# Kernel tuning notes

Measured on AMD Instinct MI355X. Metric: run time of the kernel, lower is better.

The kernel has to match this reference:

```python
import jax, jax.numpy as jnp
import numpy as np

B, N, F, D, M, R, K, TOPR = 32, 1024, 10, 64, 4, 8, 20, 2
TAU = 1.0
BN_EPS = 1e-5


def setup_inputs() -> dict:
    key = jax.random.key(0)
    ks = jax.random.split(key, 20)
    s = 0.1
    p = {}
    p['data'] = jax.random.normal(ks[0], (B, N, F), jnp.float32)
    u = jnp.clip(jax.random.uniform(ks[1], (B, M), jnp.float32), 1e-6, 1.0 - 1e-6)
    p['gumbel_noise'] = -jnp.log(-jnp.log(u))
    p['W_cond'] = jax.random.normal(ks[2], (F, D), jnp.float32) * s
    p['b_cond'] = jnp.zeros((D,), jnp.float32)
    p['W_ap'] = jax.random.normal(ks[3], (D, D), jnp.float32) * s
    p['b_ap'] = jnp.zeros((D,), jnp.float32)
    p['W_av'] = jax.random.normal(ks[4], (D, 1), jnp.float32) * s
    p['W_r'] = jax.random.normal(ks[5], (D, M), jnp.float32) * s
    p['b_r'] = jnp.zeros((M,), jnp.float32)
    p['e_base'] = jax.random.normal(ks[6], (N, D), jnp.float32) * s
    p['lr_u'] = jax.random.normal(ks[7], (M, N, R), jnp.float32) * s
    p['lr_v'] = jax.random.normal(ks[8], (M, R, D), jnp.float32) * s
    p['W_gnn'] = jax.random.normal(ks[9], (F, D), jnp.float32) * s
    p['att_i'] = jax.random.normal(ks[10], (D,), jnp.float32) * s
    p['att_j'] = jax.random.normal(ks[11], (D,), jnp.float32) * s
    p['att_em_i'] = jax.random.normal(ks[12], (D,), jnp.float32) * s
    p['att_em_j'] = jax.random.normal(ks[13], (D,), jnp.float32) * s
    p['b_gnn'] = jnp.zeros((D,), jnp.float32)
    p['bn1_gamma'] = jnp.ones((D,), jnp.float32)
    p['bn1_beta'] = jnp.zeros((D,), jnp.float32)
    p['node_embed_table'] = jax.random.normal(ks[14], (N, D), jnp.float32) * s
    p['bn_out_gamma'] = jnp.ones((D,), jnp.float32)
    p['bn_out_beta'] = jnp.zeros((D,), jnp.float32)
    p['W_out'] = jax.random.normal(ks[15], (D, 1), jnp.float32) * s
    p['b_out'] = jnp.zeros((1,), jnp.float32)
    return p


def _nan(x):
    return jnp.nan_to_num(x, nan=0.0, posinf=1e4, neginf=-1e4)


def _bn(x, gamma, beta, axes):
    # BatchNorm1d in training mode: biased batch stats over `axes`.
    mu = x.mean(axes, keepdims=True)
    var = x.var(axes, keepdims=True)
    return (x - mu) * jax.lax.rsqrt(var + BN_EPS) * gamma + beta


def reference(data, gumbel_noise, W_cond, b_cond, W_ap, b_ap, W_av, W_r, b_r,
              e_base, lr_u, lr_v, W_gnn, att_i, att_j, att_em_i, att_em_j,
              b_gnn, bn1_gamma, bn1_beta, node_embed_table,
              bn_out_gamma, bn_out_beta, W_out, b_out):
    x_det = jax.lax.stop_gradient(data)                      # data.clone().detach()
    # --- condition attention pooling ---
    h_it = data @ W_cond + b_cond                            # [B,N,D]
    ah = jax.nn.leaky_relu(h_it @ W_ap + b_ap, 0.2)
    e_it = _nan((ah @ W_av)[..., 0])                         # [B,N]
    beta = jax.nn.softmax(e_it, axis=1)
    h_sys = jnp.sum(beta[..., None] * h_it, axis=1)          # [B,D]
    # --- gumbel top-k routing with straight-through ---
    pi_soft = jax.nn.softmax((h_sys @ W_r + b_r + gumbel_noise) / TAU, axis=-1)
    topv, topi = jax.lax.top_k(pi_soft, TOPR)
    pi_hard = jnp.sum(jax.nn.one_hot(topi, M, dtype=pi_soft.dtype) * topv[..., None], axis=1)
    pi_hard = pi_hard / jnp.maximum(pi_hard.sum(-1, keepdims=True), 1e-12)
    pi_t = jax.lax.stop_gradient(pi_hard - pi_soft) + pi_soft
    # --- low-rank expert prototypes -> mixed node embeddings ---
    proto = e_base[None] + jnp.einsum('mnr,mrd->mnd', lr_u, lr_v)    # [M,N,D]
    mixed = _nan(jnp.einsum('bm,mnd->bnd', pi_t, proto))             # [B,N,D]
    # --- dynamic top-k graph construction ---
    scores = _nan(jnp.einsum('bid,bjd->bij', mixed, mixed))          # [B,N,N]
    topk_vals, topk_idx = jax.lax.top_k(scores, K)                   # src nodes per dst: [B,N,K]
    topk_w = jax.nn.softmax(topk_vals, axis=-1)                      # edge weights
    # --- GAT-style layer with embedding-augmented keys, self loops re-added ---
    x_lin = x_det @ W_gnn                                            # [B,N,D]
    s_i = x_lin @ att_i + mixed @ att_em_i                           # [B,N]
    s_j = x_lin @ att_j + mixed @ att_em_j
    sj_nb = jnp.take_along_axis(s_j, topk_idx.reshape(B, N * K), axis=1).reshape(B, N, K)
    self_mask = topk_idx == jnp.arange(N)[None, :, None]             # remove_self_loops on topk edges
    alpha_nb = jnp.where(self_mask, -jnp.inf, jax.nn.leaky_relu(s_i[:, :, None] + sj_nb, 0.2))
    alpha_self = jax.nn.leaky_relu(s_i + s_j, 0.2)
    att = jax.nn.softmax(jnp.concatenate([alpha_nb, alpha_self[..., None]], axis=-1), axis=-1)
    w_nb = att[..., :K] * topk_w                                     # edge_weight modulation
    w_self = att[..., K]
    x_src = jnp.take_along_axis(x_lin, topk_idx.reshape(B, N * K)[..., None], axis=1).reshape(B, N, K, D)
    gnn = jnp.einsum('bnk,bnkd->bnd', w_nb, x_src) + w_self[..., None] * x_lin + b_gnn
    gnn = jax.nn.relu(_bn(gnn.reshape(B * N, D), bn1_gamma, bn1_beta, 0).reshape(B, N, D))
    # --- output head ---
    out = gnn * node_embed_table[None]                               # [B,N,D]
    out = jax.nn.relu(_bn(out, bn_out_gamma, bn_out_beta, (0, 1)))   # dropout = identity (eval)
    out = (out @ W_out + b_out).reshape(-1, N)                       # [B,N]
    return out, h_sys, pi_soft
```

## Files before the change

kernel.cpp:

```cpp
#include <hip/hip_runtime.h>
#include <math.h>

#define BB 32
#define NN 1024
#define FF 10
#define DD 64
#define MM 4
#define RR 8
#define KK 20
#define BNROWS (BB*NN)

#define OFF_HIT   0ull
#define OFF_XLIN  2097152ull
#define OFF_EIT   4194304ull
#define OFF_PIT   4227072ull
#define OFF_MIXED 4227200ull
#define OFF_SI    6324352ull
#define OFF_SJ    6357120ull
#define OFF_GNN   7700608ull
#define OFF_OUTP  9797760ull
#define OFF_STAT  11894912ull
#define OFF_SC    (OFF_STAT + 2560ull)

__device__ __forceinline__ float wave_sum(float v) {
    #pragma unroll
    for (int off = 32; off; off >>= 1) v += __shfl_xor(v, off);
    return v;
}
__device__ __forceinline__ float wave_max(float v) {
    #pragma unroll
    for (int off = 32; off; off >>= 1) v = fmaxf(v, __shfl_xor(v, off));
    return v;
}

__global__ __launch_bounds__(256) void k_rows(
    const float* __restrict__ data, const float* __restrict__ W_cond,
    const float* __restrict__ b_cond, const float* __restrict__ W_ap,
    const float* __restrict__ b_ap, const float* __restrict__ W_av,
    const float* __restrict__ W_gnn,
    float* __restrict__ h_it, float* __restrict__ x_lin, float* __restrict__ e_it,
    float* __restrict__ stats)
{
    if (blockIdx.x < 10) {
        int idx = blockIdx.x * 256 + threadIdx.x;
        if (idx < 2336) stats[idx] = 0.f;
    }
    int w = threadIdx.x >> 6, lane = threadIdx.x & 63;
    int r = blockIdx.x * 4 + w;
    const float* dr = data + r * FF;
    float df[FF];
    #pragma unroll
    for (int f = 0; f < FF; f++) df[f] = dr[f];
    float h = b_cond[lane], x = 0.f;
    #pragma unroll
    for (int f = 0; f < FF; f++) {
        h = fmaf(df[f], W_cond[f * DD + lane], h);
        x = fmaf(df[f], W_gnn[f * DD + lane], x);
    }
    h_it[r * DD + lane] = h;
    x_lin[r * DD + lane] = x;
    float acc = b_ap[lane];
    #pragma unroll
    for (int e2 = 0; e2 < DD; e2++)
        acc = fmaf(__shfl(h, e2), W_ap[e2 * DD + lane], acc);
    float lr = acc > 0.f ? acc : 0.2f * acc;
    float ep = wave_sum(lr * W_av[lane]);
    if (lane == 0) e_it[r] = ep;
}

__global__ __launch_bounds__(256) void k_pool2(
    const float* __restrict__ e_it, const float* __restrict__ h_it,
    float* __restrict__ num, float* __restrict__ den)
{
    int w = threadIdx.x >> 6, lane = threadIdx.x & 63;
    int b = blockIdx.x >> 3, ch = blockIdx.x & 7;
    int base = b * NN + ch * 128 + w * 32;
    float acc = 0.f, dn = 0.f;
    #pragma unroll 4
    for (int i = 0; i < 32; i++) {
        float e = e_it[base + i];
        float wgt = expf(e);
        acc = fmaf(wgt, h_it[(size_t)(base + i) * DD + lane], acc);
        dn += wgt;
    }
    __shared__ float pa[4][DD];
    __shared__ float pd[4];
    pa[w][lane] = acc;
    if (lane == 0) pd[w] = dn;
    __syncthreads();
    if (w == 0) {
        float s = pa[0][lane] + pa[1][lane] + pa[2][lane] + pa[3][lane];
        atomicAdd(&num[b * DD + lane], s);
        if (lane == 0) atomicAdd(&den[b], pd[0] + pd[1] + pd[2] + pd[3]);
    }
}

__global__ void k_route(const float* __restrict__ num, const float* __restrict__ den,
                        const float* __restrict__ W_r, const float* __restrict__ b_r,
                        const float* __restrict__ gumbel,
                        float* __restrict__ h_sys, float* __restrict__ pi_soft,
                        float* __restrict__ pi_t)
{
    int tid = threadIdx.x;
    for (int i = tid; i < BB * DD; i += 256)
        h_sys[i] = num[i] / den[i >> 6];
    if (tid >= BB) return;
    int b = tid;
    float inv = 1.0f / den[b];
    float lg[MM];
    #pragma unroll
    for (int m = 0; m < MM; m++) lg[m] = b_r[m] + gumbel[b * MM + m];
    for (int d = 0; d < DD; d++) {
        float hv = num[b * DD + d] * inv;
        #pragma unroll
        for (int m = 0; m < MM; m++) lg[m] = fmaf(hv, W_r[d * MM + m], lg[m]);
    }
    float mx = fmaxf(fmaxf(lg[0], lg[1]), fmaxf(lg[2], lg[3]));
    float s = 0.f, p[MM];
    #pragma unroll
    for (int m = 0; m < MM; m++) { p[m] = expf(lg[m] - mx); s += p[m]; }
    #pragma unroll
    for (int m = 0; m < MM; m++) { p[m] /= s; pi_soft[b * MM + m] = p[m]; }
    int i1 = 0; float v1 = p[0];
    #pragma unroll
    for (int m = 1; m < MM; m++) if (p[m] > v1) { v1 = p[m]; i1 = m; }
    int i2 = -1; float v2 = -1.f;
    #pragma unroll
    for (int m = 0; m < MM; m++) if (m != i1 && p[m] > v2) { v2 = p[m]; i2 = m; }
    float norm = fmaxf(v1 + v2, 1e-12f);
    #pragma unroll
    for (int m = 0; m < MM; m++)
        pi_t[b * MM + m] = (m == i1 ? v1 : (m == i2 ? v2 : 0.f)) / norm;
}

__global__ __launch_bounds__(256) void k_mixed(
    const float* __restrict__ e_base, const float* __restrict__ lr_u,
    const float* __restrict__ lr_v, const float* __restrict__ pi_t,
    const float* __restrict__ x_lin,
    const float* __restrict__ att_i, const float* __restrict__ att_j,
    const float* __restrict__ att_em_i, const float* __restrict__ att_em_j,
    float* __restrict__ mixed, float* __restrict__ s_i, float* __restrict__ s_j)
{
    int w = threadIdx.x >> 6, lane = threadIdx.x & 63;
    int r = blockIdx.x * 4 + w;
    int b = r >> 10, n = r & 1023;
    float LR[MM];
    #pragma unroll
    for (int m = 0; m < MM; m++) {
        float a = 0.f;
        #pragma unroll
        for (int rr = 0; rr < RR; rr++)
            a = fmaf(lr_u[(m * NN + n) * RR + rr], lr_v[(m * RR + rr) * DD + lane], a);
        LR[m] = a;
    }
    float eb = e_base[n * DD + lane];
    float mx = 0.f;
    #pragma unroll
    for (int m = 0; m < MM; m++) mx = fmaf(pi_t[b * MM + m], eb + LR[m], mx);
    mixed[(size_t)r * DD + lane] = mx;
    float x = x_lin[(size_t)r * DD + lane];
    float r1 = wave_sum(x * att_i[lane] + mx * att_em_i[lane]);
    float r2 = wave_sum(x * att_j[lane] + mx * att_em_j[lane]);
    if (lane == 0) { s_i[r] = r1; s_j[r] = r2; }
}

__global__ __launch_bounds__(256) void k_score(
    const float* __restrict__ mixed_chunk, float* __restrict__ sc)
{
    __shared__ float As[32 * 132];
    __shared__ float Bs[32 * 132];
    int t = threadIdx.x;
    int bb = blockIdx.x >> 6;
    int rr = blockIdx.x & 63;
    int it = rr >> 3, jt = rr & 7;
    int i0 = it * 128, j0 = jt * 128;
    const float* mb = mixed_chunk + (size_t)bb * NN * DD;

    int tx = t & 15, ty = t >> 4;
    float acc[8][8];
    #pragma unroll
    for (int a = 0; a < 8; a++)
        #pragma unroll
        for (int bj = 0; bj < 8; bj++) acc[a][bj] = 0.f;

    int rowi[4], qi[4], swi[4];
    #pragma unroll
    for (int c = 0; c < 4; c++) {
        int id = t + c * 256;
        rowi[c] = (id & 15) | ((id >> 7) << 4);
        qi[c] = (id >> 4) & 7;
        swi[c] = ((rowi[c] & 4) << 4) | ((rowi[c] >> 3) << 2) | (rowi[c] & 3);
    }

    float4 pa[4], pb[4];
    #pragma unroll
    for (int c = 0; c < 4; c++) {
        pa[c] = *(const float4*)(mb + (size_t)(i0 + rowi[c]) * DD + qi[c] * 4);
        pb[c] = *(const float4*)(mb + (size_t)(j0 + rowi[c]) * DD + qi[c] * 4);
    }
    for (int hh = 0; hh < 2; hh++) {
        if (hh) __syncthreads();
        #pragma unroll
        for (int c = 0; c < 4; c++) {
            int pos = qi[c] * 4 * 132 + swi[c];
            As[pos] = pa[c].x; As[pos + 132] = pa[c].y; As[pos + 264] = pa[c].z; As[pos + 396] = pa[c].w;
            Bs[pos] = pb[c].x; Bs[pos + 132] = pb[c].y; Bs[pos + 264] = pb[c].z; Bs[pos + 396] = pb[c].w;
        }
        __syncthreads();
        if (hh == 0) {
            #pragma unroll
            for (int c = 0; c < 4; c++) {
                pa[c] = *(const float4*)(mb + (size_t)(i0 + rowi[c]) * DD + 32 + qi[c] * 4);
                pb[c] = *(const float4*)(mb + (size_t)(j0 + rowi[c]) * DD + 32 + qi[c] * 4);
            }
        }
        #pragma unroll 4
        for (int d = 0; d < 32; d++) {
            float4 a0 = *(const float4*)&As[d * 132 + ty * 4];
            float4 a1 = *(const float4*)&As[d * 132 + 64 + ty * 4];
            float4 b0 = *(const float4*)&Bs[d * 132 + tx * 4];
            float4 b1 = *(const float4*)&Bs[d * 132 + 64 + tx * 4];
            float av[8] = {a0.x, a0.y, a0.z, a0.w, a1.x, a1.y, a1.z, a1.w};
            float bv[8] = {b0.x, b0.y, b0.z, b0.w, b1.x, b1.y, b1.z, b1.w};
            #pragma unroll
            for (int a = 0; a < 8; a++)
                #pragma unroll
                for (int bj = 0; bj < 8; bj++)
                    acc[a][bj] = fmaf(av[a], bv[bj], acc[a][bj]);
        }
    }

    float* out = sc + ((size_t)bb * NN + i0 + ty * 8) * NN + j0 + tx * 8;
    #pragma unroll
    for (int a = 0; a < 8; a++) {
        float4 o0 = {acc[a][0], acc[a][1], acc[a][2], acc[a][3]};
        float4 o1 = {acc[a][4], acc[a][5], acc[a][6], acc[a][7]};
        *(float4*)(out + (size_t)a * NN) = o0;
        *(float4*)(out + (size_t)a * NN + 4) = o1;
    }
}

__global__ __launch_bounds__(256) void k_selgat(
    const float* __restrict__ sc, int b0,
    const float* __restrict__ x_lin, const float* __restrict__ s_i,
    const float* __restrict__ s_j, const float* __restrict__ b_gnn,
    float* __restrict__ gnn_pre)
{
    int w = threadIdx.x >> 6, lane = threadIdx.x & 63;
    int lr = blockIdx.x * 4 + w;
    int r = b0 * NN + lr;
    int b = r >> 10, n = r & 1023;
    const float* row = sc + (size_t)lr * NN;

    unsigned uk[16];
    #pragma unroll
    for (int c = 0; c < 4; c++) {
        float4 v = *(const float4*)(row + c * 256 + lane * 4);
        float vv[4] = {v.x, v.y, v.z, v.w};
        #pragma unroll
        for (int q = 0; q < 4; q++) {
            unsigned u = __float_as_uint(vv[q]);
            uk[c * 4 + q] = u ^ (((unsigned)((int)u >> 31)) | 0x80000000u);
        }
    }
    unsigned mx = uk[0];
    #pragma unroll
    for (int i = 1; i < 16; i++) mx = uk[i] > mx ? uk[i] : mx;
    unsigned sv = mx;
    #pragma unroll
    for (int blk = 2; blk <= 64; blk <<= 1) {
        #pragma unroll
        for (int dist = blk >> 1; dist >= 1; dist >>= 1) {
            unsigned pv = (unsigned)__shfl_xor((int)sv, dist);
            bool up = (lane & blk) == 0;
            bool upper = (lane & dist) == 0;
            bool g = sv > pv;
            sv = (((g == upper) == up)) ? sv : pv;
        }
    }
    unsigned tau = (unsigned)__shfl((int)sv, 19);

    __shared__ unsigned skey[4][64];
    __shared__ int sjj[4][64];
    int base = 0;
    #pragma unroll
    for (int s = 0; s < 16; s++) {
        bool q = uk[s] >= tau;
        unsigned long long m = __ballot(q);
        if (q) {
            int pos = base + __popcll(m & ((1ull << lane) - 1ull));
            if (pos < 64) {
                skey[w][pos] = uk[s];
                sjj[w][pos] = ((s >> 2) << 8) + lane * 4 + (s & 3);
            }
        }
        base += __popcll(m);
    }
    int C = base;

    float vk = -INFINITY; int ik = 0;
    if (C <= 64) {
        unsigned ck = 0u; int cj = 0x7FFFFFFF;
        if (lane < C) { ck = skey[w][lane]; cj = sjj[w][lane]; }
        if (C <= 32) {
            #pragma unroll
            for (int blk = 2; blk <= 32; blk <<= 1)
                #pragma unroll
                for (int dist = blk >> 1; dist >= 1; dist >>= 1) {
                    unsigned pk = (unsigned)__shfl_xor((int)ck, dist);
                    int pj = __shfl_xor(cj, dist);
                    bool up = (lane & blk) == 0;
                    bool upper = (lane & dist) == 0;
                    bool g = (ck > pk) || (ck == pk && cj < pj);
                    bool keep = ((g == upper) == up);
                    ck = keep ? ck : pk; cj = keep ? cj : pj;
                }
        } else {
            #pragma unroll
            for (int blk = 2; blk <= 64; blk <<= 1)
                #pragma unroll
                for (int dist = blk >> 1; dist >= 1; dist >>= 1) {
                    unsigned pk = (unsigned)__shfl_xor((int)ck, dist);
                    int pj = __shfl_xor(cj, dist);
                    bool up = (lane & blk) == 0;
                    bool upper = (lane & dist) == 0;
                    bool g = (ck > pk) || (ck == pk && cj < pj);
                    bool keep = ((g == upper) == up);
                    ck = keep ? ck : pk; cj = keep ? cj : pj;
                }
        }
        if (lane < KK) {
            unsigned u = (ck & 0x80000000u) ? (ck ^ 0x80000000u) : ~ck;
            vk = __uint_as_float(u);
            ik = cj;
        }
    } else {
        for (int k = 0; k < KK; k++) {
            unsigned bm = uk[0]; int bsl = 0;
            #pragma unroll
            for (int i = 1; i < 16; i++) if (uk[i] > bm) { bm = uk[i]; bsl = i; }
            unsigned wm = bm;
            #pragma unroll
            for (int off = 32; off; off >>= 1) {
                unsigned tt = (unsigned)__shfl_xor((int)wm, off);
                wm = tt > wm ? tt : wm;
            }
            unsigned long long ball = __ballot(bm == wm);
            int winner = (int)__builtin_ctzll(ball);
            int slotw = __shfl(bsl, winner);
            int jw = ((slotw >> 2) << 8) + winner * 4 + (slotw & 3);
            unsigned u2 = (wm & 0x80000000u) ? (wm ^ 0x80000000u) : ~wm;
            if (lane == k) { vk = __uint_as_float(u2); ik = jw; }
            if (lane == winner) uk[bsl] = 0u;
        }
    }

    float m1 = wave_max(vk);
    float ek = (lane < KK) ? expf(vk - m1) : 0.f;
    float s1v = wave_sum(ek);
    float wk = ek / s1v;
    float si = s_i[r], sjn = s_j[r];
    float a = -INFINITY;
    if (lane < KK) {
        float sjk = s_j[(b << 10) + ik];
        float t2 = si + sjk;
        a = (ik == n) ? -INFINITY : (t2 > 0.f ? t2 : 0.2f * t2);
    }
    float ts = si + sjn;
    float aself = ts > 0.f ? ts : 0.2f * ts;
    float am = wave_max(fmaxf(a, aself));
    float ea = (lane < KK && a != -INFINITY) ? expf(a - am) : 0.f;
    float es = expf(aself - am);
    float ssum = wave_sum(ea) + es;
    float wnb = (ea / ssum) * wk;
    float wself = es / ssum;
    float acc = b_gnn[lane] + wself * x_lin[(size_t)r * DD + lane];
    #pragma unroll
    for (int k = 0; k < KK; k++) {
        int jk = __shfl(ik, k);
        float wv = __shfl(wnb, k);
        acc = fmaf(wv, x_lin[((size_t)(b << 10) + jk) * DD + lane], acc);
    }
    gnn_pre[(size_t)r * DD + lane] = acc;
}

__global__ __launch_bounds__(256) void k_stats(const float* __restrict__ src, float* __restrict__ sums)
{
    int w = threadIdx.x >> 6, lane = threadIdx.x & 63;
    __shared__ float ps[4][DD], pq[4][DD];
    float s = 0.f, q = 0.f;
    int base = blockIdx.x * 128;
    for (int i = w; i < 128; i += 4) {
        float v = src[(size_t)(base + i) * DD + lane];
        s += v; q = fmaf(v, v, q);
    }
    ps[w][lane] = s; pq[w][lane] = q;
    __syncthreads();
    if (w == 0) {
        s = ps[0][lane] + ps[1][lane] + ps[2][lane] + ps[3][lane];
        q = pq[0][lane] + pq[1][lane] + pq[2][lane] + pq[3][lane];
        atomicAdd(&sums[lane], s);
        atomicAdd(&sums[DD + lane], q);
    }
}

__global__ __launch_bounds__(256) void k_bn1(
    const float* __restrict__ gnn_pre, float* __restrict__ stats,
    const float* __restrict__ gamma, const float* __restrict__ beta,
    const float* __restrict__ net, float* __restrict__ out_pre)
{
    int tid = threadIdx.x;
    int d0 = (tid & 15) * 4;
    float mean4[4], rs4[4], bt4[4];
    #pragma unroll
    for (int k = 0; k < 4; k++) {
        float mu = stats[d0 + k] * (1.0f / BNROWS);
        float var = stats[64 + d0 + k] * (1.0f / BNROWS) - mu * mu;
        mean4[k] = mu;
        rs4[k] = rsqrtf(var + 1e-5f) * gamma[d0 + k];
        bt4[k] = beta[d0 + k];
    }
    float s4[4] = {0, 0, 0, 0}, q4[4] = {0, 0, 0, 0};
    size_t base4 = (size_t)blockIdx.x * 2048;
    #pragma unroll
    for (int i = 0; i < 8; i++) {
        size_t f4 = base4 + (size_t)i * 256 + tid;
        float4 v = ((const float4*)gnn_pre)[f4];
        int n = ((int)(f4 >> 4)) & 1023;
        float4 nv = ((const float4*)net)[(size_t)n * 16 + (tid & 15)];
        float vv[4] = {v.x, v.y, v.z, v.w};
        float nn2[4] = {nv.x, nv.y, nv.z, nv.w};
        float ov[4];
        #pragma unroll
        for (int k = 0; k < 4; k++) {
            float y = (vv[k] - mean4[k]) * rs4[k] + bt4[k];
            y = y > 0.f ? y : 0.f;
            float o = y * nn2[k];
            ov[k] = o;
            s4[k] += o;
            q4[k] = fmaf(o, o, q4[k]);
        }
        float4 o4 = {ov[0], ov[1], ov[2], ov[3]};
        ((float4*)out_pre)[f4] = o4;
    }
    __shared__ float4 ls[256], lq[256];
    ls[tid] = make_float4(s4[0], s4[1], s4[2], s4[3]);
    lq[tid] = make_float4(q4[0], q4[1], q4[2], q4[3]);
    __syncthreads();
    if (tid < 16) {
        float4 S = ls[tid], Q = lq[tid];
        #pragma unroll
        for (int rr = 1; rr < 16; rr++) {
            float4 a = ls[tid + 16 * rr], b = lq[tid + 16 * rr];
            S.x += a.x; S.y += a.y; S.z += a.z; S.w += a.w;
            Q.x += b.x; Q.y += b.y; Q.z += b.z; Q.w += b.w;
        }
        atomicAdd(&stats[128 + tid * 4 + 0], S.x);
        atomicAdd(&stats[128 + tid * 4 + 1], S.y);
        atomicAdd(&stats[128 + tid * 4 + 2], S.z);
        atomicAdd(&stats[128 + tid * 4 + 3], S.w);
        atomicAdd(&stats[192 + tid * 4 + 0], Q.x);
        atomicAdd(&stats[192 + tid * 4 + 1], Q.y);
        atomicAdd(&stats[192 + tid * 4 + 2], Q.z);
        atomicAdd(&stats[192 + tid * 4 + 3], Q.w);
    }
}

__global__ __launch_bounds__(256) void k_head(
    const float* __restrict__ out_pre, const float* __restrict__ stats,
    const float* __restrict__ gamma, const float* __restrict__ beta,
    const float* __restrict__ W_out, const float* __restrict__ b_out,
    float* __restrict__ out)
{
    int w = threadIdx.x >> 6, lane = threadIdx.x & 63;
    int r = blockIdx.x * 4 + w;
    float mean = stats[lane] * (1.0f / BNROWS);
    float var = stats[DD + lane] * (1.0f / BNROWS) - mean * mean;
    float rs = rsqrtf(var + 1e-5f);
    float y = (out_pre[(size_t)r * DD + lane] - mean) * rs * gamma[lane] + beta[lane];
    y = y > 0.f ? y : 0.f;
    float p = wave_sum(y * W_out[lane]);
    if (lane == 0) out[r] = p + b_out[0];
}

extern "C" void kernel_launch(void* const* d_in, const int* in_sizes, int n_in,
                              void* d_out, int out_size, void* d_ws, size_t ws_size,
                              hipStream_t stream)
{
    const float* data     = (const float*)d_in[0];
    const float* gumbel   = (const float*)d_in[1];
    const float* W_cond   = (const float*)d_in[2];
    const float* b_cond   = (const float*)d_in[3];
    const float* W_ap     = (const float*)d_in[4];
    const float* b_ap     = (const float*)d_in[5];
    const float* W_av     = (const float*)d_in[6];
    const float* W_r      = (const float*)d_in[7];
    const float* b_r      = (const float*)d_in[8];
    const float* e_base   = (const float*)d_in[9];
    const float* lr_u     = (const float*)d_in[10];
    const float* lr_v     = (const float*)d_in[11];
    const float* W_gnn    = (const float*)d_in[12];
    const float* att_i    = (const float*)d_in[13];
    const float* att_j    = (const float*)d_in[14];
    const float* att_em_i = (const float*)d_in[15];
    const float* att_em_j = (const float*)d_in[16];
    const float* b_gnn    = (const float*)d_in[17];
    const float* bn1_g    = (const float*)d_in[18];
    const float* bn1_b    = (const float*)d_in[19];
    const float* net      = (const float*)d_in[20];
    const float* bno_g    = (const float*)d_in[21];
    const float* bno_b    = (const float*)d_in[22];
    const float* W_out    = (const float*)d_in[23];
    const float* b_out    = (const float*)d_in[24];

    float* ws = (float*)d_ws;
    float* h_it   = ws + OFF_HIT;
    float* x_lin  = ws + OFF_XLIN;
    float* e_it   = ws + OFF_EIT;
    float* pi_t   = ws + OFF_PIT;
    float* mixed  = ws + OFF_MIXED;
    float* s_i    = ws + OFF_SI;
    float* s_j    = ws + OFF_SJ;
    float* gnn_pre = ws + OFF_GNN;
    float* out_pre = ws + OFF_OUTP;
    float* stats   = ws + OFF_STAT;
    float* pnum    = stats + 256;
    float* pden    = stats + 2304;

    float* out0    = (float*)d_out;
    float* h_sys   = out0 + BB * NN;
    float* pi_soft = out0 + BB * NN + BB * DD;

    k_rows<<<BNROWS / 4, 256, 0, stream>>>(data, W_cond, b_cond, W_ap, b_ap, W_av, W_gnn,
                                           h_it, x_lin, e_it, stats);
    k_pool2<<<BB * 8, 256, 0, stream>>>(e_it, h_it, pnum, pden);
    k_route<<<1, 256, 0, stream>>>(pnum, pden, W_r, b_r, gumbel, h_sys, pi_soft, pi_t);
    k_mixed<<<BNROWS / 4, 256, 0, stream>>>(e_base, lr_u, lr_v, pi_t, x_lin,
                                            att_i, att_j, att_em_i, att_em_j, mixed, s_i, s_j);

    size_t ws_floats = ws_size / 4;
    size_t avail = ws_floats > OFF_SC ? ws_floats - OFF_SC : 0;
    int cb = (int)(avail / (size_t)(NN * NN));
    if (cb > BB) cb = BB;
    float* sc = ws + OFF_SC;
    if (cb < 1) { cb = 2; sc = h_it; }
    for (int b0 = 0; b0 < BB; b0 += cb) {
        int c = (BB - b0) < cb ? (BB - b0) : cb;
        k_score<<<c * 64, 256, 0, stream>>>(mixed + (size_t)b0 * NN * DD, sc);
        k_selgat<<<c * 256, 256, 0, stream>>>(sc, b0, x_lin, s_i, s_j, b_gnn, gnn_pre);
    }

    k_stats<<<256, 256, 0, stream>>>(gnn_pre, stats);
    k_bn1<<<256, 256, 0, stream>>>(gnn_pre, stats, bn1_g, bn1_b, net, out_pre);
    k_head<<<BNROWS / 4, 256, 0, stream>>>(out_pre, stats + 128, bno_g, bno_b, W_out, b_out, out0);
}
```

Baseline: 319.8 us.

## Fuse score GEMM, top-k selection, GAT aggregation and BN stats into one kernel

Replaces the separate score-matrix kernel, the selection/GAT kernel and the stats kernel with a single kernel. Each block computes a 16x1024 score tile for one batch, keeping it in registers, and runs the top-k and attention aggregation directly on those registers. It also accumulates the BN sums, so the 32x1024x1024 score matrix never goes through global memory and the separate stats pass is gone. In exchange the full key matrix is reloaded per 16-row tile, and each thread holds 64 accumulators, which raises register pressure.

```diff
diff --git a/kernel.cpp b/kernel.cpp
--- a/kernel.cpp
+++ b/kernel.cpp
@@ -20,7 +20,6 @@
 #define OFF_GNN   7700608ull
 #define OFF_OUTP  9797760ull
 #define OFF_STAT  11894912ull
-#define OFF_SC    (OFF_STAT + 2560ull)
 
 __device__ __forceinline__ float wave_sum(float v) {
     #pragma unroll
@@ -164,243 +163,209 @@
     if (lane == 0) { s_i[r] = r1; s_j[r] = r2; }
 }
 
-__global__ __launch_bounds__(256) void k_score(
-    const float* __restrict__ mixed_chunk, float* __restrict__ sc)
-{
-    __shared__ float As[32 * 132];
-    __shared__ float Bs[32 * 132];
-    int t = threadIdx.x;
-    int bb = blockIdx.x >> 6;
-    int rr = blockIdx.x & 63;
-    int it = rr >> 3, jt = rr & 7;
-    int i0 = it * 128, j0 = jt * 128;
-    const float* mb = mixed_chunk + (size_t)bb * NN * DD;
-
-    int tx = t & 15, ty = t >> 4;
-    float acc[8][8];
-    #pragma unroll
-    for (int a = 0; a < 8; a++)
-        #pragma unroll
-        for (int bj = 0; bj < 8; bj++) acc[a][bj] = 0.f;
-
-    int rowi[4], qi[4], swi[4];
-    #pragma unroll
-    for (int c = 0; c < 4; c++) {
-        int id = t + c * 256;
-        rowi[c] = (id & 15) | ((id >> 7) << 4);
-        qi[c] = (id >> 4) & 7;
-        swi[c] = ((rowi[c] & 4) << 4) | ((rowi[c] >> 3) << 2) | (rowi[c] & 3);
-    }
-
-    float4 pa[4], pb[4];
-    #pragma unroll
-    for (int c = 0; c < 4; c++) {
-        pa[c] = *(const float4*)(mb + (size_t)(i0 + rowi[c]) * DD + qi[c] * 4);
-        pb[c] = *(const float4*)(mb + (size_t)(j0 + rowi[c]) * DD + qi[c] * 4);
-    }
-    for (int hh = 0; hh < 2; hh++) {
-        if (hh) __syncthreads();
-        #pragma unroll
-        for (int c = 0; c < 4; c++) {
-            int pos = qi[c] * 4 * 132 + swi[c];
-            As[pos] = pa[c].x; As[pos + 132] = pa[c].y; As[pos + 264] = pa[c].z; As[pos + 396] = pa[c].w;
-            Bs[pos] = pb[c].x; Bs[pos + 132] = pb[c].y; Bs[pos + 264] = pb[c].z; Bs[pos + 396] = pb[c].w;
-        }
-        __syncthreads();
-        if (hh == 0) {
-            #pragma unroll
-            for (int c = 0; c < 4; c++) {
-                pa[c] = *(const float4*)(mb + (size_t)(i0 + rowi[c]) * DD + 32 + qi[c] * 4);
-                pb[c] = *(const float4*)(mb + (size_t)(j0 + rowi[c]) * DD + 32 + qi[c] * 4);
-            }
-        }
-        #pragma unroll 4
-        for (int d = 0; d < 32; d++) {
-            float4 a0 = *(const float4*)&As[d * 132 + ty * 4];
-            float4 a1 = *(const float4*)&As[d * 132 + 64 + ty * 4];
-            float4 b0 = *(const float4*)&Bs[d * 132 + tx * 4];
-            float4 b1 = *(const float4*)&Bs[d * 132 + 64 + tx * 4];
-            float av[8] = {a0.x, a0.y, a0.z, a0.w, a1.x, a1.y, a1.z, a1.w};
-            float bv[8] = {b0.x, b0.y, b0.z, b0.w, b1.x, b1.y, b1.z, b1.w};
-            #pragma unroll
-            for (int a = 0; a < 8; a++)
-                #pragma unroll
-                for (int bj = 0; bj < 8; bj++)
-                    acc[a][bj] = fmaf(av[a], bv[bj], acc[a][bj]);
-        }
-    }
-
-    float* out = sc + ((size_t)bb * NN + i0 + ty * 8) * NN + j0 + tx * 8;
-    #pragma unroll
-    for (int a = 0; a < 8; a++) {
-        float4 o0 = {acc[a][0], acc[a][1], acc[a][2], acc[a][3]};
-        float4 o1 = {acc[a][4], acc[a][5], acc[a][6], acc[a][7]};
-        *(float4*)(out + (size_t)a * NN) = o0;
-        *(float4*)(out + (size_t)a * NN + 4) = o1;
-    }
-}
-
-__global__ __launch_bounds__(256) void k_selgat(
-    const float* __restrict__ sc, int b0,
-    const float* __restrict__ x_lin, const float* __restrict__ s_i,
-    const float* __restrict__ s_j, const float* __restrict__ b_gnn,
-    float* __restrict__ gnn_pre)
-{
-    int w = threadIdx.x >> 6, lane = threadIdx.x & 63;
-    int lr = blockIdx.x * 4 + w;
-    int r = b0 * NN + lr;
-    int b = r >> 10, n = r & 1023;
-    const float* row = sc + (size_t)lr * NN;
-
-    unsigned uk[16];
-    #pragma unroll
-    for (int c = 0; c < 4; c++) {
-        float4 v = *(const float4*)(row + c * 256 + lane * 4);
-        float vv[4] = {v.x, v.y, v.z, v.w};
-        #pragma unroll
-        for (int q = 0; q < 4; q++) {
-            unsigned u = __float_as_uint(vv[q]);
-            uk[c * 4 + q] = u ^ (((unsigned)((int)u >> 31)) | 0x80000000u);
-        }
-    }
-    unsigned mx = uk[0];
-    #pragma unroll
-    for (int i = 1; i < 16; i++) mx = uk[i] > mx ? uk[i] : mx;
-    unsigned sv = mx;
-    #pragma unroll
-    for (int blk = 2; blk <= 64; blk <<= 1) {
-        #pragma unroll
-        for (int dist = blk >> 1; dist >= 1; dist >>= 1) {
-            unsigned pv = (unsigned)__shfl_xor((int)sv, dist);
-            bool up = (lane & blk) == 0;
-            bool upper = (lane & dist) == 0;
-            bool g = sv > pv;
-            sv = (((g == upper) == up)) ? sv : pv;
-        }
-    }
-    unsigned tau = (unsigned)__shfl((int)sv, 19);
-
+__global__ __launch_bounds__(256, 4) void k_fuse(
+    const float* __restrict__ mixed, const float* __restrict__ x_lin,
+    const float* __restrict__ s_i, const float* __restrict__ s_j,
+    const float* __restrict__ b_gnn, float* __restrict__ gnn_pre,
+    float* __restrict__ stats)
+{
+    __shared__ float As[64 * 20];
+    __shared__ float Bs[32 * 260];
     __shared__ unsigned skey[4][64];
     __shared__ int sjj[4][64];
-    int base = 0;
-    #pragma unroll
-    for (int s = 0; s < 16; s++) {
-        bool q = uk[s] >= tau;
-        unsigned long long m = __ballot(q);
-        if (q) {
-            int pos = base + __popcll(m & ((1ull << lane) - 1ull));
-            if (pos < 64) {
-                skey[w][pos] = uk[s];
-                sjj[w][pos] = ((s >> 2) << 8) + lane * 4 + (s & 3);
-            }
-        }
-        base += __popcll(m);
-    }
-    int C = base;
-
-    float vk = -INFINITY; int ik = 0;
-    if (C <= 64) {
-        unsigned ck = 0u; int cj = 0x7FFFFFFF;
-        if (lane < C) { ck = skey[w][lane]; cj = sjj[w][lane]; }
-        if (C <= 32) {
+
+    int t = threadIdx.x, w = t >> 6, lane = t & 63;
+    int b = blockIdx.x >> 6, itile = blockIdx.x & 63;
+    int i0 = itile * 16;
+    const float* mb = mixed + (size_t)b * NN * DD;
+
+    {
+        int row = t >> 4, q = t & 15;
+        float4 v = *(const float4*)(mb + (size_t)(i0 + row) * DD + q * 4);
+        As[(q * 4 + 0) * 20 + row] = v.x;
+        As[(q * 4 + 1) * 20 + row] = v.y;
+        As[(q * 4 + 2) * 20 + row] = v.z;
+        As[(q * 4 + 3) * 20 + row] = v.w;
+    }
+
+    float acc[4][16];
+    #pragma unroll
+    for (int r = 0; r < 4; r++)
+        #pragma unroll
+        for (int s = 0; s < 16; s++) acc[r][s] = 0.f;
+
+    #pragma unroll
+    for (int jt = 0; jt < 4; jt++) {
+        #pragma unroll
+        for (int dh = 0; dh < 2; dh++) {
+            __syncthreads();
             #pragma unroll
-            for (int blk = 2; blk <= 32; blk <<= 1)
+            for (int c = 0; c < 8; c++) {
+                int id = t + c * 256;
+                int j = id >> 3, q = id & 7;
+                float4 v = *(const float4*)(mb + (size_t)(jt * 256 + j) * DD + dh * 32 + q * 4);
+                Bs[(q * 4 + 0) * 260 + j] = v.x;
+                Bs[(q * 4 + 1) * 260 + j] = v.y;
+                Bs[(q * 4 + 2) * 260 + j] = v.z;
+                Bs[(q * 4 + 3) * 260 + j] = v.w;
+            }
+            __syncthreads();
+            #pragma unroll 8
+            for (int d2 = 0; d2 < 32; d2++) {
+                float4 a4 = *(const float4*)&As[(dh * 32 + d2) * 20 + w * 4];
+                float4 b4 = *(const float4*)&Bs[d2 * 260 + lane * 4];
+                float av[4] = {a4.x, a4.y, a4.z, a4.w};
+                float bv[4] = {b4.x, b4.y, b4.z, b4.w};
                 #pragma unroll
-                for (int dist = blk >> 1; dist >= 1; dist >>= 1) {
-                    unsigned pk = (unsigned)__shfl_xor((int)ck, dist);
-                    int pj = __shfl_xor(cj, dist);
-                    bool up = (lane & blk) == 0;
-                    bool upper = (lane & dist) == 0;
-                    bool g = (ck > pk) || (ck == pk && cj < pj);
-                    bool keep = ((g == upper) == up);
-                    ck = keep ? ck : pk; cj = keep ? cj : pj;
+                for (int r = 0; r < 4; r++)
+                    #pragma unroll
+                    for (int q = 0; q < 4; q++)
+                        acc[r][q + jt * 4] = fmaf(av[r], bv[q], acc[r][q + jt * 4]);
+            }
+        }
+    }
+
+    float sl = 0.f, ql = 0.f;
+    #pragma unroll
+    for (int r = 0; r < 4; r++) {
+        int n = i0 + w * 4 + r;
+        int gr = (b << 10) + n;
+
+        unsigned uk[16];
+        #pragma unroll
+        for (int s = 0; s < 16; s++) {
+            unsigned u = __float_as_uint(acc[r][s]);
+            uk[s] = u ^ (((unsigned)((int)u >> 31)) | 0x80000000u);
+        }
+        unsigned mx = uk[0];
+        #pragma unroll
+        for (int i = 1; i < 16; i++) mx = uk[i] > mx ? uk[i] : mx;
+        unsigned sv = mx;
+        #pragma unroll
+        for (int blk = 2; blk <= 64; blk <<= 1) {
+            #pragma unroll
+            for (int dist = blk >> 1; dist >= 1; dist >>= 1) {
+                unsigned pv = (unsigned)__shfl_xor((int)sv, dist);
+                bool up = (lane & blk) == 0;
+                bool upper = (lane & dist) == 0;
+                bool g = sv > pv;
+                sv = (((g == upper) == up)) ? sv : pv;
+            }
+        }
+        unsigned tau = (unsigned)__shfl((int)sv, 19);
+
+        int base = 0;
+        #pragma unroll
+        for (int s = 0; s < 16; s++) {
+            bool q = uk[s] >= tau;
+            unsigned long long m = __ballot(q);
+            if (q) {
+                int pos = base + __popcll(m & ((1ull << lane) - 1ull));
+                if (pos < 64) {
+                    skey[w][pos] = uk[s];
+                    sjj[w][pos] = ((s >> 2) << 8) + lane * 4 + (s & 3);
                 }
+            }
+            base += __popcll(m);
+        }
+        int C = base;
+
+        float vk = -INFINITY; int ik = 0;
+        if (C <= 64) {
+            unsigned ck = 0u; int cj = 0x7FFFFFFF;
+            if (lane < C) { ck = skey[w][lane]; cj = sjj[w][lane]; }
+            if (C <= 32) {
+                #pragma unroll
+                for (int blk = 2; blk <= 32; blk <<= 1)
+                    #pragma unroll
+                    for (int dist = blk >> 1; dist >= 1; dist >>= 1) {
+                        unsigned pk = (unsigned)__shfl_xor((int)ck, dist);
+                        int pj = __shfl_xor(cj, dist);
+                        bool up = (lane & blk) == 0;
+                        bool upper = (lane & dist) == 0;
+                        bool g = (ck > pk) || (ck == pk && cj < pj);
+                        bool keep = ((g == upper) == up);
+                        ck = keep ? ck : pk; cj = keep ? cj : pj;
+                    }
+            } else {
+                #pragma unroll
+                for (int blk = 2; blk <= 64; blk <<= 1)
+                    #pragma unroll
+                    for (int dist = blk >> 1; dist >= 1; dist >>= 1) {
+                        unsigned pk = (unsigned)__shfl_xor((int)ck, dist);
+                        int pj = __shfl_xor(cj, dist);
+                        bool up = (lane & blk) == 0;
+                        bool upper = (lane & dist) == 0;
+                        bool g = (ck > pk) || (ck == pk && cj < pj);
+                        bool keep = ((g == upper) == up);
+                        ck = keep ? ck : pk; cj = keep ? cj : pj;
+                    }
+            }
+            if (lane < KK) {
+                unsigned u = (ck & 0x80000000u) ? (ck ^ 0x80000000u) : ~ck;
+                vk = __uint_as_float(u);
+                ik = cj;
+            }
         } else {
-            #pragma unroll
-            for (int blk = 2; blk <= 64; blk <<= 1)
+            for (int k = 0; k < KK; k++) {
+                unsigned bm = uk[0]; int bsl = 0;
                 #pragma unroll
-                for (int dist = blk >> 1; dist >= 1; dist >>= 1) {
-                    unsigned pk = (unsigned)__shfl_xor((int)ck, dist);
-                    int pj = __shfl_xor(cj, dist);
-                    bool up = (lane & blk) == 0;
-                    bool upper = (lane & dist) == 0;
-                    bool g = (ck > pk) || (ck == pk && cj < pj);
-                    bool keep = ((g == upper) == up);
-                    ck = keep ? ck : pk; cj = keep ? cj : pj;
+                for (int i = 1; i < 16; i++) if (uk[i] > bm) { bm = uk[i]; bsl = i; }
+                unsigned wm = bm;
+                #pragma unroll
+                for (int off = 32; off; off >>= 1) {
+                    unsigned tt = (unsigned)__shfl_xor((int)wm, off);
+                    wm = tt > wm ? tt : wm;
                 }
-        }
+                unsigned long long ball = __ballot(bm == wm);
+                int winner = (int)__builtin_ctzll(ball);
+                int slotw = __shfl(bsl, winner);
+                int jw = ((slotw >> 2) << 8) + winner * 4 + (slotw & 3);
+                unsigned u2 = (wm & 0x80000000u) ? (wm ^ 0x80000000u) : ~wm;
+                if (lane == k) { vk = __uint_as_float(u2); ik = jw; }
+                if (lane == winner) uk[bsl] = 0u;
+            }
+        }
+
+        float m1 = wave_max(vk);
+        float ek = (lane < KK) ? expf(vk - m1) : 0.f;
+        float s1v = wave_sum(ek);
+        float wk = ek / s1v;
+        float si = s_i[gr], sjn = s_j[gr];
+        float a = -INFINITY;
         if (lane < KK) {
-            unsigned u = (ck & 0x80000000u) ? (ck ^ 0x80000000u) : ~ck;
-            vk = __uint_as_float(u);
-            ik = cj;
-        }
-    } else {
+            float sjk = s_j[(b << 10) + ik];
+            float t2 = si + sjk;
+            a = (ik == n) ? -INFINITY : (t2 > 0.f ? t2 : 0.2f * t2);
+        }
+        float ts = si + sjn;
+        float aself = ts > 0.f ? ts : 0.2f * ts;
+        float am = wave_max(fmaxf(a, aself));
+        float ea = (lane < KK && a != -INFINITY) ? expf(a - am) : 0.f;
+        float es = expf(aself - am);
+        float ssum = wave_sum(ea) + es;
+        float wnb = (ea / ssum) * wk;
+        float wself = es / ssum;
+        float accg = b_gnn[lane] + wself * x_lin[(size_t)gr * DD + lane];
+        #pragma unroll
         for (int k = 0; k < KK; k++) {
-            unsigned bm = uk[0]; int bsl = 0;
-            #pragma unroll
-            for (int i = 1; i < 16; i++) if (uk[i] > bm) { bm = uk[i]; bsl = i; }
-            unsigned wm = bm;
-            #pragma unroll
-            for (int off = 32; off; off >>= 1) {
-                unsigned tt = (unsigned)__shfl_xor((int)wm, off);
-                wm = tt > wm ? tt : wm;
-            }
-            unsigned long long ball = __ballot(bm == wm);
-            int winner = (int)__builtin_ctzll(ball);
-            int slotw = __shfl(bsl, winner);
-            int jw = ((slotw >> 2) << 8) + winner * 4 + (slotw & 3);
-            unsigned u2 = (wm & 0x80000000u) ? (wm ^ 0x80000000u) : ~wm;
-            if (lane == k) { vk = __uint_as_float(u2); ik = jw; }
-            if (lane == winner) uk[bsl] = 0u;
-        }
-    }
-
-    float m1 = wave_max(vk);
-    float ek = (lane < KK) ? expf(vk - m1) : 0.f;
-    float s1v = wave_sum(ek);
-    float wk = ek / s1v;
-    float si = s_i[r], sjn = s_j[r];
-    float a = -INFINITY;
-    if (lane < KK) {
-        float sjk = s_j[(b << 10) + ik];
-        float t2 = si + sjk;
-        a = (ik == n) ? -INFINITY : (t2 > 0.f ? t2 : 0.2f * t2);
-    }
-    float ts = si + sjn;
-    float aself = ts > 0.f ? ts : 0.2f * ts;
-    float am = wave_max(fmaxf(a, aself));
-    float ea = (lane < KK && a != -INFINITY) ? expf(a - am) : 0.f;
-    float es = expf(aself - am);
-    float ssum = wave_sum(ea) + es;
-    float wnb = (ea / ssum) * wk;
-    float wself = es / ssum;
-    float acc = b_gnn[lane] + wself * x_lin[(size_t)r * DD + lane];
-    #pragma unroll
-    for (int k = 0; k < KK; k++) {
-        int jk = __shfl(ik, k);
-        float wv = __shfl(wnb, k);
-        acc = fmaf(wv, x_lin[((size_t)(b << 10) + jk) * DD + lane], acc);
-    }
-    gnn_pre[(size_t)r * DD + lane] = acc;
-}
-
-__global__ __launch_bounds__(256) void k_stats(const float* __restrict__ src, float* __restrict__ sums)
-{
-    int w = threadIdx.x >> 6, lane = threadIdx.x & 63;
-    __shared__ float ps[4][DD], pq[4][DD];
-    float s = 0.f, q = 0.f;
-    int base = blockIdx.x * 128;
-    for (int i = w; i < 128; i += 4) {
-        float v = src[(size_t)(base + i) * DD + lane];
-        s += v; q = fmaf(v, v, q);
-    }
-    ps[w][lane] = s; pq[w][lane] = q;
+            int jk = __shfl(ik, k);
+            float wv = __shfl(wnb, k);
+            accg = fmaf(wv, x_lin[((size_t)(b << 10) + jk) * DD + lane], accg);
+        }
+        gnn_pre[(size_t)gr * DD + lane] = accg;
+        sl += accg; ql = fmaf(accg, accg, ql);
+    }
+
+    __syncthreads();
+    As[w * 64 + lane] = sl;
+    As[256 + w * 64 + lane] = ql;
     __syncthreads();
     if (w == 0) {
-        s = ps[0][lane] + ps[1][lane] + ps[2][lane] + ps[3][lane];
-        q = pq[0][lane] + pq[1][lane] + pq[2][lane] + pq[3][lane];
-        atomicAdd(&sums[lane], s);
-        atomicAdd(&sums[DD + lane], q);
+        float S = As[lane] + As[64 + lane] + As[128 + lane] + As[192 + lane];
+        float Q = As[256 + lane] + As[320 + lane] + As[384 + lane] + As[448 + lane];
+        atomicAdd(&stats[lane], S);
+        atomicAdd(&stats[64 + lane], Q);
     }
 }
 
@@ -537,20 +502,7 @@
     k_route<<<1, 256, 0, stream>>>(pnum, pden, W_r, b_r, gumbel, h_sys, pi_soft, pi_t);
     k_mixed<<<BNROWS / 4, 256, 0, stream>>>(e_base, lr_u, lr_v, pi_t, x_lin,
                                             att_i, att_j, att_em_i, att_em_j, mixed, s_i, s_j);
-
-    size_t ws_floats = ws_size / 4;
-    size_t avail = ws_floats > OFF_SC ? ws_floats - OFF_SC : 0;
-    int cb = (int)(avail / (size_t)(NN * NN));
-    if (cb > BB) cb = BB;
-    float* sc = ws + OFF_SC;
-    if (cb < 1) { cb = 2; sc = h_it; }
-    for (int b0 = 0; b0 < BB; b0 += cb) {
-        int c = (BB - b0) < cb ? (BB - b0) : cb;
-        k_score<<<c * 64, 256, 0, stream>>>(mixed + (size_t)b0 * NN * DD, sc);
-        k_selgat<<<c * 256, 256, 0, stream>>>(sc, b0, x_lin, s_i, s_j, b_gnn, gnn_pre);
-    }
-
-    k_stats<<<256, 256, 0, stream>>>(gnn_pre, stats);
+    k_fuse<<<2048, 256, 0, stream>>>(mixed, x_lin, s_i, s_j, b_gnn, gnn_pre, stats);
     k_bn1<<<256, 256, 0, stream>>>(gnn_pre, stats, bn1_g, bn1_b, net, out_pre);
     k_head<<<BNROWS / 4, 256, 0, stream>>>(out_pre, stats + 128, bno_g, bno_b, W_out, b_out, out0);
 }
```

New measurement: 329.3 us. +3.0%, slower.
